# Kernel tuning notes

Hardware: AMD Instinct MI355X
Metric: run time of the kernel (lower is better)

The kernel has to match this reference:

```python
import jax, jax.numpy as jnp
import numpy as np

N, E, D, H, C, HID, ED = 50000, 800000, 128, 8, 16, 512, 32


def setup_inputs() -> dict:
    key = jax.random.key(0)
    ks = jax.random.split(key, 16)
    s = 0.05
    return {
        "h": jax.random.normal(ks[0], (N, D), jnp.float32),
        "edge_index": jax.random.randint(ks[1], (2, E), 0, N, jnp.int64),
        "edge_attr": jax.random.normal(ks[2], (E, ED), jnp.float32),
        "w1": jax.random.normal(ks[3], (D, HID), jnp.float32) * s,
        "b1": jnp.zeros((HID,), jnp.float32),
        "w2": jax.random.normal(ks[4], (HID, D), jnp.float32) * s,
        "b2": jnp.zeros((D,), jnp.float32),
        "ln_g": jnp.ones((D,), jnp.float32),
        "ln_b": jnp.zeros((D,), jnp.float32),
        "Wl": jax.random.normal(ks[5], (D, H * C), jnp.float32) * s,
        "bl": jnp.zeros((H * C,), jnp.float32),
        "Wr": jax.random.normal(ks[6], (D, H * C), jnp.float32) * s,
        "br": jnp.zeros((H * C,), jnp.float32),
        "We": jax.random.normal(ks[7], (ED, H * C), jnp.float32) * s,
        "att": jax.random.normal(ks[8], (H, C), jnp.float32) * s,
        "bias_out": jnp.zeros((H * C,), jnp.float32),
    }


def _layer_norm(x, g, b, eps=1e-5):
    mu = jnp.mean(x, axis=-1, keepdims=True)
    var = jnp.var(x, axis=-1, keepdims=True)
    return (x - mu) * jax.lax.rsqrt(var + eps) * g + b


def reference(h, edge_index, edge_attr, w1, b1, w2, b2, ln_g, ln_b,
              Wl, bl, Wr, br, We, att, bias_out):
    # FFN + residual + LayerNorm (dropout = identity in eval)
    u = jax.nn.relu(h @ w1 + b1) @ w2 + b2
    v = _layer_norm(h + u, ln_g, ln_b)

    src, dst = edge_index[0], edge_index[1]
    # GATv2Conv: separate source/target transforms + edge transform
    xl = (v @ Wl + bl).reshape(N, H, C)
    xr = (v @ Wr + br).reshape(N, H, C)
    xe = (edge_attr @ We).reshape(E, H, C)
    x = jax.nn.leaky_relu(xl[src] + xr[dst] + xe, 0.2)  # [E,H,C]
    logits = jnp.einsum("ehc,hc->eh", x, att)            # [E,H]
    # segment softmax over incoming edges of each destination node
    m = jax.lax.stop_gradient(jax.ops.segment_max(logits, dst, num_segments=N))
    ex = jnp.exp(logits - m[dst])
    den = jax.ops.segment_sum(ex, dst, num_segments=N)
    alpha = ex / den[dst]                                # [E,H]
    msg = xl[src] * alpha[..., None]                     # [E,H,C]
    w = jax.ops.segment_sum(msg, dst, num_segments=N).reshape(N, H * C) + bias_out
    output = _layer_norm(w + v, ln_g, ln_b)
    return output, alpha
```

## Files before the change

kernel.cpp:

```cpp
#include <hip/hip_runtime.h>
#include <math.h>

#define N_NODES 50000
#define E_EDGES 800000
#define D_DIM   128
#define H_HEADS 8
#define C_CH    16
#define HID_DIM 512
#define ED_DIM  32

typedef __attribute__((ext_vector_type(8))) short short8;
typedef __attribute__((ext_vector_type(4))) float f32x4;

__device__ __forceinline__ short f2bf(float f) {
    unsigned u = __float_as_uint(f);
    return (short)((u + 0x7FFFu + ((u >> 16) & 1u)) >> 16);
}
__device__ __forceinline__ float bf2f(short s) {
    return __uint_as_float(((unsigned)(unsigned short)s) << 16);
}

__global__ __launch_bounds__(64) void repack_kernel(
    const float* __restrict__ w1, const float* __restrict__ w2,
    const float* __restrict__ Wl, const float* __restrict__ Wr,
    const float* __restrict__ We,
    short8* __restrict__ w1p, short8* __restrict__ w2p,
    short8* __restrict__ Wlp, short8* __restrict__ Wrp,
    short8* __restrict__ Wep)
{
    int b = blockIdx.x;
    const float* src; short8* dst; int Nw, nc, rel;
    if (b < 128)      { src = w1; dst = w1p; Nw = 512; nc = 4;  rel = b; }
    else if (b < 256) { src = w2; dst = w2p; Nw = 128; nc = 16; rel = b - 128; }
    else if (b < 288) { src = Wl; dst = Wlp; Nw = 128; nc = 4;  rel = b - 256; }
    else if (b < 320) { src = Wr; dst = Wrp; Nw = 128; nc = 4;  rel = b - 288; }
    else              { src = We; dst = Wep; Nw = 128; nc = 1;  rel = b - 320; }
    int t = rel / nc, c = rel % nc;
    int l = threadIdx.x, quad = l >> 4, col = l & 15;
    short8 r;
    #pragma unroll
    for (int j = 0; j < 8; ++j)
        r[j] = f2bf(src[(size_t)(c * 32 + quad * 8 + j) * Nw + t * 16 + col]);
    dst[(size_t)rel * 64 + l] = r;
}

__global__ __launch_bounds__(256) void count_kernel(
    const int* __restrict__ edge_index, unsigned* __restrict__ cnt,
    unsigned short* __restrict__ rank)
{
    int e = blockIdx.x * 256 + threadIdx.x;
    int dst = edge_index[E_EDGES + e];
    rank[e] = (unsigned short)atomicAdd(&cnt[dst], 1u);
}

__global__ __launch_bounds__(256) void node_ffn_mfma(
    const float* __restrict__ h,
    const float* __restrict__ b1, const float* __restrict__ b2,
    const float* __restrict__ ln_g, const float* __restrict__ ln_b,
    const float* __restrict__ bl, const float* __restrict__ br,
    const short8* __restrict__ w1p, const short8* __restrict__ w2p,
    const short8* __restrict__ Wlp, const short8* __restrict__ Wrp,
    float* __restrict__ v_out,
    unsigned short* __restrict__ xl_bf_out, unsigned short* __restrict__ xr_bf_out)
{
    __shared__ short hid_bf[16 * 520];
    __shared__ float v_s[16 * 132];
    __shared__ short v_bf[16 * 136];

    const int tid = threadIdx.x;
    const int w = tid >> 6, lane = tid & 63;
    const int m = lane & 15, quad = lane >> 4;
    const int n0 = blockIdx.x * 16;

    short8 af[4];
    #pragma unroll
    for (int c = 0; c < 4; ++c) {
        const float* hp = h + (size_t)(n0 + m) * 128 + c * 32 + quad * 8;
        float4 p0 = ((const float4*)hp)[0];
        float4 p1 = ((const float4*)hp)[1];
        short8 a;
        a[0] = f2bf(p0.x); a[1] = f2bf(p0.y); a[2] = f2bf(p0.z); a[3] = f2bf(p0.w);
        a[4] = f2bf(p1.x); a[5] = f2bf(p1.y); a[6] = f2bf(p1.z); a[7] = f2bf(p1.w);
        af[c] = a;
    }

    {
        f32x4 acc[8];
        #pragma unroll
        for (int t = 0; t < 8; ++t) acc[t] = (f32x4){0.f, 0.f, 0.f, 0.f};
        #pragma unroll
        for (int t = 0; t < 8; ++t) {
            int tile = w * 8 + t;
            #pragma unroll
            for (int c = 0; c < 4; ++c) {
                short8 bf = w1p[(size_t)(tile * 4 + c) * 64 + lane];
                acc[t] = __builtin_amdgcn_mfma_f32_16x16x32_bf16(af[c], bf, acc[t], 0, 0, 0);
            }
        }
        #pragma unroll
        for (int t = 0; t < 8; ++t) {
            int col = (w * 8 + t) * 16 + m;
            float bias = b1[col];
            #pragma unroll
            for (int r = 0; r < 4; ++r) {
                int row = quad * 4 + r;
                hid_bf[row * 520 + col] = f2bf(fmaxf(acc[t][r] + bias, 0.f));
            }
        }
    }
    __syncthreads();

    {
        f32x4 acc2[2];
        acc2[0] = (f32x4){0.f, 0.f, 0.f, 0.f};
        acc2[1] = (f32x4){0.f, 0.f, 0.f, 0.f};
        #pragma unroll 4
        for (int c = 0; c < 16; ++c) {
            short8 a = *(const short8*)&hid_bf[m * 520 + c * 32 + quad * 8];
            #pragma unroll
            for (int t = 0; t < 2; ++t) {
                short8 bf = w2p[(size_t)((w * 2 + t) * 16 + c) * 64 + lane];
                acc2[t] = __builtin_amdgcn_mfma_f32_16x16x32_bf16(a, bf, acc2[t], 0, 0, 0);
            }
        }
        #pragma unroll
        for (int t = 0; t < 2; ++t) {
            int col = (w * 2 + t) * 16 + m;
            float bias = b2[col];
            #pragma unroll
            for (int r = 0; r < 4; ++r) {
                int row = quad * 4 + r;
                v_s[row * 132 + col] = acc2[t][r] + bias + h[(size_t)(n0 + row) * 128 + col];
            }
        }
    }
    __syncthreads();

    {
        float g0 = ln_g[lane], g1 = ln_g[lane + 64];
        float be0 = ln_b[lane], be1 = ln_b[lane + 64];
        #pragma unroll
        for (int p = 0; p < 4; ++p) {
            int nd = w * 4 + p;
            float x0 = v_s[nd * 132 + lane], x1 = v_s[nd * 132 + lane + 64];
            float s = x0 + x1, ss = x0 * x0 + x1 * x1;
            #pragma unroll
            for (int off = 1; off < 64; off <<= 1) {
                s  += __shfl_xor(s, off);
                ss += __shfl_xor(ss, off);
            }
            float mu = s * (1.f / 128.f);
            float var = ss * (1.f / 128.f) - mu * mu;
            float rs = rsqrtf(var + 1e-5f);
            float y0 = (x0 - mu) * rs * g0 + be0;
            float y1 = (x1 - mu) * rs * g1 + be1;
            v_out[(size_t)(n0 + nd) * 128 + lane]      = y0;
            v_out[(size_t)(n0 + nd) * 128 + lane + 64] = y1;
            v_bf[nd * 136 + lane]      = f2bf(y0);
            v_bf[nd * 136 + lane + 64] = f2bf(y1);
        }
    }
    __syncthreads();

    {
        short8 af3[4];
        #pragma unroll
        for (int c = 0; c < 4; ++c)
            af3[c] = *(const short8*)&v_bf[m * 136 + c * 32 + quad * 8];
        f32x4 accl[2], accr[2];
        #pragma unroll
        for (int t = 0; t < 2; ++t) {
            accl[t] = (f32x4){0.f, 0.f, 0.f, 0.f};
            accr[t] = (f32x4){0.f, 0.f, 0.f, 0.f};
        }
        #pragma unroll
        for (int t = 0; t < 2; ++t) {
            int tile = w * 2 + t;
            #pragma unroll
            for (int c = 0; c < 4; ++c) {
                accl[t] = __builtin_amdgcn_mfma_f32_16x16x32_bf16(
                    af3[c], Wlp[(size_t)(tile * 4 + c) * 64 + lane], accl[t], 0, 0, 0);
                accr[t] = __builtin_amdgcn_mfma_f32_16x16x32_bf16(
                    af3[c], Wrp[(size_t)(tile * 4 + c) * 64 + lane], accr[t], 0, 0, 0);
            }
        }
        #pragma unroll
        for (int t = 0; t < 2; ++t) {
            int col = (w * 2 + t) * 16 + m;
            float bld = bl[col], brd = br[col];
            #pragma unroll
            for (int r = 0; r < 4; ++r) {
                int row = quad * 4 + r;
                xl_bf_out[(size_t)(n0 + row) * 128 + col] = (unsigned short)f2bf(accl[t][r] + bld);
                xr_bf_out[(size_t)(n0 + row) * 128 + col] = (unsigned short)f2bf(accr[t][r] + brd);
            }
        }
    }
}

__global__ __launch_bounds__(1024) void scan_kernel(
    const unsigned* __restrict__ cnt, int* __restrict__ rowstart)
{
    __shared__ int wsum[16];
    const int t = threadIdx.x, wv = t >> 6, lane = t & 63;
    const int base4 = t * 13;
    int4 v[13];
    int lsum = 0;
    #pragma unroll
    for (int k = 0; k < 13; ++k) {
        int i4 = base4 + k;
        int4 x = make_int4(0, 0, 0, 0);
        if (i4 < N_NODES / 4) x = ((const int4*)cnt)[i4];
        v[k] = x;
        lsum += x.x + x.y + x.z + x.w;
    }
    int s = lsum;
    #pragma unroll
    for (int off = 1; off < 64; off <<= 1) {
        int nb = __shfl_up(s, off);
        if (lane >= off) s += nb;
    }
    if (lane == 63) wsum[wv] = s;
    __syncthreads();
    int woff = 0;
    for (int k = 0; k < wv; ++k) woff += wsum[k];
    int run = woff + s - lsum;
    #pragma unroll
    for (int k = 0; k < 13; ++k) {
        int i4 = base4 + k;
        if (i4 < N_NODES / 4) {
            int4 r;
            r.x = run; run += v[k].x;
            r.y = run; run += v[k].y;
            r.z = run; run += v[k].z;
            r.w = run; run += v[k].w;
            ((int4*)rowstart)[i4] = r;
        }
    }
}

__global__ __launch_bounds__(256) void scatter_kernel(
    const int* __restrict__ edge_index, const unsigned short* __restrict__ rank,
    const int* __restrict__ rowstart, int* __restrict__ eidx,
    unsigned* __restrict__ srcdst)
{
    int e = blockIdx.x * 256 + threadIdx.x;
    if (e >= E_EDGES) return;
    int src = edge_index[e];
    int dst = edge_index[E_EDGES + e];
    int pos = rowstart[dst] + (int)rank[e];
    eidx[pos] = e;
    srcdst[pos] = (unsigned)src | ((unsigned)dst << 16);
}

__global__ __launch_bounds__(256) void edge_logits_mfma(
    const int* __restrict__ eidx, const unsigned* __restrict__ srcdst,
    const float* __restrict__ edge_attr,
    const short8* __restrict__ Wep, const float* __restrict__ att,
    const unsigned short* __restrict__ xl_bf, const unsigned short* __restrict__ xr_bf,
    float* __restrict__ exbuf)
{
    __shared__ short8 We_f[512];
    __shared__ short xe_s[64 * 136];
    __shared__ int e_s[64];
    __shared__ unsigned sd_s[64];
    const int tid = threadIdx.x;
    const int w = tid >> 6, lane = tid & 63;
    const int m = lane & 15, quad = lane >> 4;
    const int p0b = blockIdx.x * 64;

    We_f[tid]       = Wep[tid];
    We_f[tid + 256] = Wep[tid + 256];
    if (tid < 64) {
        int pos = p0b + tid;
        e_s[tid]  = eidx[pos];
        sd_s[tid] = srcdst[pos];
    }
    __syncthreads();

    const float* eap = edge_attr + (size_t)e_s[w * 16 + m] * 32 + quad * 8;
    float4 p0 = ((const float4*)eap)[0];
    float4 p1 = ((const float4*)eap)[1];
    short8 a;
    a[0] = f2bf(p0.x); a[1] = f2bf(p0.y); a[2] = f2bf(p0.z); a[3] = f2bf(p0.w);
    a[4] = f2bf(p1.x); a[5] = f2bf(p1.y); a[6] = f2bf(p1.z); a[7] = f2bf(p1.w);

    f32x4 acc[8];
    #pragma unroll
    for (int t = 0; t < 8; ++t) acc[t] = (f32x4){0.f, 0.f, 0.f, 0.f};
    #pragma unroll
    for (int t = 0; t < 8; ++t)
        acc[t] = __builtin_amdgcn_mfma_f32_16x16x32_bf16(a, We_f[t * 64 + lane], acc[t], 0, 0, 0);

    #pragma unroll
    for (int t = 0; t < 8; ++t) {
        #pragma unroll
        for (int r = 0; r < 4; ++r)
            xe_s[(w * 16 + quad * 4 + r) * 136 + t * 16 + m] = f2bf(acc[t][r]);
    }
    __syncthreads();

    const int g = quad;
    const int s = m;
    const int d0 = s * 8;
    float4 at0 = ((const float4*)(att + d0))[0];
    float4 at1 = ((const float4*)(att + d0))[1];

    #pragma unroll
    for (int p = 0; p < 4; ++p) {
        int el = p * 16 + w * 4 + g;
        unsigned sd = sd_s[el];
        int src = (int)(sd & 0xffffu);
        int dst = (int)(sd >> 16);
        short8 xl8 = *(const short8*)&xl_bf[(size_t)src * 128 + d0];
        short8 xr8 = *(const short8*)&xr_bf[(size_t)dst * 128 + d0];
        short8 xe8 = *(const short8*)&xe_s[el * 136 + d0];

        float atv[8] = { at0.x, at0.y, at0.z, at0.w, at1.x, at1.y, at1.z, at1.w };
        float pq = 0.f;
        #pragma unroll
        for (int dd = 0; dd < 8; ++dd) {
            float x = bf2f(xl8[dd]) + bf2f(xr8[dd]) + bf2f(xe8[dd]);
            x = (x > 0.f) ? x : 0.2f * x;
            pq += x * atv[dd];
        }
        pq += __shfl_xor(pq, 1);
        if ((s & 1) == 0)
            exbuf[(size_t)(p0b + el) * 8 + (s >> 1)] = expf(pq);
    }
}

__global__ __launch_bounds__(256) void node_aggregate_kernel(
    const int* __restrict__ eidx, const int* __restrict__ rowstart,
    const unsigned* __restrict__ cnt, const unsigned* __restrict__ srcdst,
    const float* __restrict__ exbuf,
    const unsigned short* __restrict__ xl_bf, const float* __restrict__ v,
    const float* __restrict__ bias_out,
    const float* __restrict__ ln_g, const float* __restrict__ ln_b,
    float* __restrict__ alpha_out, float* __restrict__ out)
{
    const int wv = threadIdx.x >> 6, lane = threadIdx.x & 63;
    const int n = blockIdx.x * 4 + wv;
    if (n >= N_NODES) return;
    const int start = rowstart[n];
    const int num = (int)cnt[n];

    const int g = lane >> 4, s = lane & 15;
    const int h3 = s >> 1;
    float acc[8] = {0.f, 0.f, 0.f, 0.f, 0.f, 0.f, 0.f, 0.f};
    float den = 0.f;

    int i = 0;
    for (; i + 8 <= num; i += 8) {
        int pos0 = start + i + g;
        int pos1 = pos0 + 4;
        unsigned sda = srcdst[pos0];
        unsigned sdb = srcdst[pos1];
        float exa = exbuf[(size_t)pos0 * 8 + h3];
        float exb = exbuf[(size_t)pos1 * 8 + h3];
        short8 qa = *(const short8*)&xl_bf[(size_t)(sda & 0xffffu) * 128 + s * 8];
        short8 qb = *(const short8*)&xl_bf[(size_t)(sdb & 0xffffu) * 128 + s * 8];
        if ((s & 1) == 0) den += exa + exb;
        #pragma unroll
        for (int k = 0; k < 8; ++k) {
            acc[k] += bf2f(qa[k]) * exa;
            acc[k] += bf2f(qb[k]) * exb;
        }
    }
    for (; i < num; i += 4) {
        int ii = i + g;
        if (ii < num) {
            int pos = start + ii;
            int src = (int)(srcdst[pos] & 0xffffu);
            float ex = exbuf[(size_t)pos * 8 + h3];
            if ((s & 1) == 0) den += ex;
            short8 q = *(const short8*)&xl_bf[(size_t)src * 128 + s * 8];
            #pragma unroll
            for (int k = 0; k < 8; ++k) acc[k] += bf2f(q[k]) * ex;
        }
    }
    #pragma unroll
    for (int k = 0; k < 8; ++k) {
        acc[k] += __shfl_xor(acc[k], 16);
        acc[k] += __shfl_xor(acc[k], 32);
    }
    den += __shfl_xor(den, 16);
    den += __shfl_xor(den, 32);
    float den_h = __shfl(den, 2 * h3);
    float inv = (num > 0) ? (1.f / den_h) : 0.f;

    const float* vp = v + (size_t)n * 128 + s * 8;
    float4 v0 = ((const float4*)vp)[0], v1 = ((const float4*)vp)[1];
    float4 b0 = ((const float4*)(bias_out + s * 8))[0];
    float4 b1 = ((const float4*)(bias_out + s * 8))[1];
    float x[8];
    x[0] = acc[0] * inv + b0.x + v0.x; x[1] = acc[1] * inv + b0.y + v0.y;
    x[2] = acc[2] * inv + b0.z + v0.z; x[3] = acc[3] * inv + b0.w + v0.w;
    x[4] = acc[4] * inv + b1.x + v1.x; x[5] = acc[5] * inv + b1.y + v1.y;
    x[6] = acc[6] * inv + b1.z + v1.z; x[7] = acc[7] * inv + b1.w + v1.w;
    float sm = 0.f, ssm = 0.f;
    #pragma unroll
    for (int k = 0; k < 8; ++k) { sm += x[k]; ssm += x[k] * x[k]; }
    #pragma unroll
    for (int off = 1; off < 16; off <<= 1) {
        sm  += __shfl_xor(sm, off);
        ssm += __shfl_xor(ssm, off);
    }
    float mu = sm * (1.f / 128.f);
    float var = ssm * (1.f / 128.f) - mu * mu;
    float rs = rsqrtf(var + 1e-5f);
    if (g == 0) {
        float4 g0 = ((const float4*)(ln_g + s * 8))[0];
        float4 g1 = ((const float4*)(ln_g + s * 8))[1];
        float4 be0 = ((const float4*)(ln_b + s * 8))[0];
        float4 be1 = ((const float4*)(ln_b + s * 8))[1];
        float4 o0, o1;
        o0.x = (x[0] - mu) * rs * g0.x + be0.x;
        o0.y = (x[1] - mu) * rs * g0.y + be0.y;
        o0.z = (x[2] - mu) * rs * g0.z + be0.z;
        o0.w = (x[3] - mu) * rs * g0.w + be0.w;
        o1.x = (x[4] - mu) * rs * g1.x + be1.x;
        o1.y = (x[5] - mu) * rs * g1.y + be1.y;
        o1.z = (x[6] - mu) * rs * g1.z + be1.z;
        o1.w = (x[7] - mu) * rs * g1.w + be1.w;
        float4* op = (float4*)(out + (size_t)n * 128 + s * 8);
        op[0] = o0; op[1] = o1;
    }

    if (num > 0) {
        const int h7 = lane & 7, j8 = lane >> 3;
        float invh = __shfl(inv, 2 * h7);
        for (int i2 = j8; i2 < num; i2 += 8) {
            int pos = start + i2;
            float ex = exbuf[(size_t)pos * 8 + h7];
            int e = eidx[pos];
            alpha_out[(size_t)e * 8 + h7] = ex * invh;
        }
    }
}

extern "C" void kernel_launch(void* const* d_in, const int* in_sizes, int n_in,
                              void* d_out, int out_size, void* d_ws, size_t ws_size,
                              hipStream_t stream)
{
    const float* h        = (const float*)d_in[0];
    const int*   edge_idx = (const int*)  d_in[1];
    const float* edge_attr= (const float*)d_in[2];
    const float* w1       = (const float*)d_in[3];
    const float* b1       = (const float*)d_in[4];
    const float* w2       = (const float*)d_in[5];
    const float* b2       = (const float*)d_in[6];
    const float* ln_g     = (const float*)d_in[7];
    const float* ln_b     = (const float*)d_in[8];
    const float* Wl       = (const float*)d_in[9];
    const float* bl       = (const float*)d_in[10];
    const float* Wr       = (const float*)d_in[11];
    const float* br       = (const float*)d_in[12];
    const float* We       = (const float*)d_in[13];
    const float* att      = (const float*)d_in[14];
    const float* bias_out = (const float*)d_in[15];

    float* out   = (float*)d_out;
    float* alpha = out + (size_t)N_NODES * 128;

    short8* w1p = (short8*)alpha;
    short8* w2p = w1p + 128 * 64;
    short8* Wlp = w2p + 128 * 64;
    short8* Wrp = Wlp + 32 * 64;

    float*          v        = (float*)d_ws;
    unsigned short* xl_bf    = (unsigned short*)(v + (size_t)N_NODES*128);
    unsigned short* xr_bf    = xl_bf + (size_t)N_NODES * 128;
    float*          exbuf    = (float*)(xr_bf + (size_t)N_NODES * 128);
    unsigned*       cnt      = (unsigned*)(exbuf + (size_t)E_EDGES * 8);
    int*            rowstart = (int*)(cnt + N_NODES);
    unsigned short* rank     = (unsigned short*)(rowstart + N_NODES);
    short8*         Wep      = (short8*)(rank + E_EDGES);
    int*            eidx     = (int*)(Wep + 512);
    unsigned*       srcdst   = (unsigned*)(eidx + E_EDGES);

    hipMemsetAsync(cnt, 0, (size_t)N_NODES * sizeof(unsigned), stream);

    repack_kernel<<<328, 64, 0, stream>>>(w1, w2, Wl, Wr, We,
                                          w1p, w2p, Wlp, Wrp, Wep);
    count_kernel<<<E_EDGES / 256, 256, 0, stream>>>(edge_idx, cnt, rank);
    node_ffn_mfma<<<N_NODES / 16, 256, 0, stream>>>(
        h, b1, b2, ln_g, ln_b, bl, br, w1p, w2p, Wlp, Wrp, v, xl_bf, xr_bf);
    scan_kernel<<<1, 1024, 0, stream>>>(cnt, rowstart);
    scatter_kernel<<<(E_EDGES + 255) / 256, 256, 0, stream>>>(
        edge_idx, rank, rowstart, eidx, srcdst);
    edge_logits_mfma<<<E_EDGES / 64, 256, 0, stream>>>(
        eidx, srcdst, edge_attr, Wep, att, xl_bf, xr_bf, exbuf);
    node_aggregate_kernel<<<(N_NODES + 3) / 4, 256, 0, stream>>>(
        eidx, rowstart, cnt, srcdst, exbuf, xl_bf, v, bias_out, ln_g, ln_b, alpha, out);
}
```

Baseline: 436.2 us.

## Permute We columns so edge MFMA outputs feed logits directly from registers

The We weight repack is permuted so that each MFMA output column lines up with the 8 contiguous channels a lane later uses for the attention dot product. The edge-logit kernel can then use the accumulator registers directly, dropping the xe shared-memory staging buffer, one block barrier, and the shared staging of edge indices. It also switches to fmaxf for leaky ReLU and to fast __expf. This lowers LDS use and likely raises occupancy, at the cost of per-lane global loads of srcdst and slightly less exact exponentials.

```diff
diff --git a/kernel.cpp b/kernel.cpp
--- a/kernel.cpp
+++ b/kernel.cpp
@@ -30,17 +30,22 @@
 {
     int b = blockIdx.x;
     const float* src; short8* dst; int Nw, nc, rel;
+    bool perm = false;
     if (b < 128)      { src = w1; dst = w1p; Nw = 512; nc = 4;  rel = b; }
     else if (b < 256) { src = w2; dst = w2p; Nw = 128; nc = 16; rel = b - 128; }
     else if (b < 288) { src = Wl; dst = Wlp; Nw = 128; nc = 4;  rel = b - 256; }
     else if (b < 320) { src = Wr; dst = Wrp; Nw = 128; nc = 4;  rel = b - 288; }
-    else              { src = We; dst = Wep; Nw = 128; nc = 1;  rel = b - 320; }
+    else              { src = We; dst = Wep; Nw = 128; nc = 1;  rel = b - 320; perm = true; }
     int t = rel / nc, c = rel % nc;
     int l = threadIdx.x, quad = l >> 4, col = l & 15;
     short8 r;
     #pragma unroll
-    for (int j = 0; j < 8; ++j)
-        r[j] = f2bf(src[(size_t)(c * 32 + quad * 8 + j) * Nw + t * 16 + col]);
+    for (int j = 0; j < 8; ++j) {
+        if (perm)
+            r[j] = f2bf(src[(size_t)(quad * 8 + j) * 128 + col * 8 + t]);
+        else
+            r[j] = f2bf(src[(size_t)(c * 32 + quad * 8 + j) * Nw + t * 16 + col]);
+    }
     dst[(size_t)rel * 64 + l] = r;
 }
 
@@ -261,9 +266,6 @@
     float* __restrict__ exbuf)
 {
     __shared__ short8 We_f[512];
-    __shared__ short xe_s[64 * 136];
-    __shared__ int e_s[64];
-    __shared__ unsigned sd_s[64];
     const int tid = threadIdx.x;
     const int w = tid >> 6, lane = tid & 63;
     const int m = lane & 15, quad = lane >> 4;
@@ -271,20 +273,17 @@
 
     We_f[tid]       = Wep[tid];
     We_f[tid + 256] = Wep[tid + 256];
-    if (tid < 64) {
-        int pos = p0b + tid;
-        e_s[tid]  = eidx[pos];
-        sd_s[tid] = srcdst[pos];
-    }
-    __syncthreads();
-
-    const float* eap = edge_attr + (size_t)e_s[w * 16 + m] * 32 + quad * 8;
+
+    int em = eidx[p0b + w * 16 + m];
+    const float* eap = edge_attr + (size_t)em * 32 + quad * 8;
     float4 p0 = ((const float4*)eap)[0];
     float4 p1 = ((const float4*)eap)[1];
     short8 a;
     a[0] = f2bf(p0.x); a[1] = f2bf(p0.y); a[2] = f2bf(p0.z); a[3] = f2bf(p0.w);
     a[4] = f2bf(p1.x); a[5] = f2bf(p1.y); a[6] = f2bf(p1.z); a[7] = f2bf(p1.w);
 
+    __syncthreads();
+
     f32x4 acc[8];
     #pragma unroll
     for (int t = 0; t < 8; ++t) acc[t] = (f32x4){0.f, 0.f, 0.f, 0.f};
@@ -292,41 +291,30 @@
     for (int t = 0; t < 8; ++t)
         acc[t] = __builtin_amdgcn_mfma_f32_16x16x32_bf16(a, We_f[t * 64 + lane], acc[t], 0, 0, 0);
 
-    #pragma unroll
-    for (int t = 0; t < 8; ++t) {
-        #pragma unroll
-        for (int r = 0; r < 4; ++r)
-            xe_s[(w * 16 + quad * 4 + r) * 136 + t * 16 + m] = f2bf(acc[t][r]);
-    }
-    __syncthreads();
-
-    const int g = quad;
-    const int s = m;
-    const int d0 = s * 8;
+    const int d0 = m * 8;
     float4 at0 = ((const float4*)(att + d0))[0];
     float4 at1 = ((const float4*)(att + d0))[1];
-
-    #pragma unroll
-    for (int p = 0; p < 4; ++p) {
-        int el = p * 16 + w * 4 + g;
-        unsigned sd = sd_s[el];
+    float atv[8] = { at0.x, at0.y, at0.z, at0.w, at1.x, at1.y, at1.z, at1.w };
+
+    #pragma unroll
+    for (int r = 0; r < 4; ++r) {
+        int el = w * 16 + quad * 4 + r;
+        unsigned sd = srcdst[p0b + el];
         int src = (int)(sd & 0xffffu);
         int dst = (int)(sd >> 16);
         short8 xl8 = *(const short8*)&xl_bf[(size_t)src * 128 + d0];
         short8 xr8 = *(const short8*)&xr_bf[(size_t)dst * 128 + d0];
-        short8 xe8 = *(const short8*)&xe_s[el * 136 + d0];
-
-        float atv[8] = { at0.x, at0.y, at0.z, at0.w, at1.x, at1.y, at1.z, at1.w };
+
         float pq = 0.f;
         #pragma unroll
-        for (int dd = 0; dd < 8; ++dd) {
-            float x = bf2f(xl8[dd]) + bf2f(xr8[dd]) + bf2f(xe8[dd]);
-            x = (x > 0.f) ? x : 0.2f * x;
-            pq += x * atv[dd];
+        for (int t = 0; t < 8; ++t) {
+            float x = bf2f(xl8[t]) + bf2f(xr8[t]) + acc[t][r];
+            x = fmaxf(x, 0.2f * x);
+            pq += x * atv[t];
         }
         pq += __shfl_xor(pq, 1);
-        if ((s & 1) == 0)
-            exbuf[(size_t)(p0b + el) * 8 + (s >> 1)] = expf(pq);
+        if ((m & 1) == 0)
+            exbuf[(size_t)(p0b + el) * 8 + (m >> 1)] = __expf(pq);
     }
 }
 
```

Measured after the change: 453.0 us. 3.9% more time.
